# Optimization experiments

Measured on AMD Instinct MI355X. Metric: run time of the kernel, lower is better.

The kernel has to match this reference:

```python
import jax, jax.numpy as jnp
import numpy as np

B, D, E, H, O = 32768, 1200, 16, 1024, 1
K = 4
LN_EPS = 1e-5


def setup_inputs() -> dict:
    key = jax.random.key(0)
    ks = jax.random.split(key, 4)
    x = jax.random.normal(ks[0], (B, D), dtype=jnp.float32)
    w_gate = jax.random.normal(ks[1], (D, E), dtype=jnp.float32) * 0.05
    W1 = jax.random.normal(ks[2], (E, D, H), dtype=jnp.float32) * 0.02
    b1 = jnp.zeros((E, H), dtype=jnp.float32)
    gamma = jnp.ones((E, H), dtype=jnp.float32)
    beta = jnp.zeros((E, H), dtype=jnp.float32)
    W2 = jax.random.normal(ks[3], (E, H, O), dtype=jnp.float32) * 0.02
    b2 = jnp.zeros((E, O), dtype=jnp.float32)
    return {"x": x, "w_gate": w_gate, "W1": W1, "b1": b1,
            "gamma": gamma, "beta": beta, "W2": W2, "b2": b2, "k": K}


def _cv_squared(v):
    # torch .var() is unbiased (ddof=1)
    return jnp.var(v, ddof=1) / (jnp.mean(v) ** 2 + 1e-10)


def reference(x, w_gate, W1, b1, gamma, beta, W2, b2, k):
    nB = x.shape[0]
    nE = w_gate.shape[1]
    # --- top-k gating (eval path: no noise, dropout identity) ---
    logits = jax.nn.softmax(x @ w_gate, axis=1)               # [B, E]
    top_vals, top_idx = jax.lax.top_k(logits, min(k + 1, nE))  # [B, k+1]
    tk_v = top_vals[:, :k]                                     # [B, k]
    tk_i = top_idx[:, :k]
    tk_g = tk_v / (jnp.sum(tk_v, axis=1, keepdims=True) + 1e-6)
    gates = jnp.zeros_like(logits).at[jnp.arange(nB)[:, None], tk_i].set(tk_g)
    # --- load-balancing loss ---
    importance = gates.sum(0)
    load = (gates > 0).sum(0).astype(jnp.float32)
    loss = 0.5 * (_cv_squared(importance) + _cv_squared(load))
    # --- expert MLPs; dense per-expert compute masked by gates ---
    # (equivalent to sparse dispatch/combine: gate==0 rows contribute nothing,
    #  LayerNorm is per-row so no cross-token coupling)
    y = jnp.zeros((nB, W2.shape[-1]), dtype=jnp.float32)
    for e in range(nE):
        h = x @ W1[e] + b1[e]                                  # [B, H]
        mu = jnp.mean(h, axis=-1, keepdims=True)
        var = jnp.var(h, axis=-1, keepdims=True)               # biased, as torch LN
        h = (h - mu) / jnp.sqrt(var + LN_EPS) * gamma[e] + beta[e]
        h = jax.nn.relu(h)
        o = jax.nn.sigmoid(h @ W2[e] + b2[e])                  # [B, O]
        y = y + gates[:, e:e + 1] * o
    return y, loss
```

## Files before the change

kernel.cpp:

```cpp
#include <hip/hip_runtime.h>
#include <math.h>


#define B_SZ   32768
#define D_SZ   1200
#define DP     1216
#define E_SZ   16
#define H_SZ   1024
#define LN_EPS 1e-5f
#define BM     64
#define KBLK   32
#define NSTEP  (DP / KBLK)
#define NBG    512
#define GR     64

typedef __attribute__((ext_vector_type(8))) short  short8;
typedef __attribute__((ext_vector_type(4))) float  f32x4;

__device__ __forceinline__ unsigned short f2bf(float f) {
    unsigned u = __float_as_uint(f);
    unsigned r = u + 0x7FFFu + ((u >> 16) & 1u);
    return (unsigned short)(r >> 16);
}

__device__ __forceinline__ void gload_lds16(const void* g, void* l) {
    __builtin_amdgcn_global_load_lds(
        (const __attribute__((address_space(1))) void*)g,
        (__attribute__((address_space(3))) void*)l, 16, 0, 0);
}

__global__ __launch_bounds__(256)
void gate_a(const float* __restrict__ x, const float* __restrict__ wg,
            unsigned* __restrict__ tk_pack, float* __restrict__ gates4,
            unsigned short* __restrict__ lpos4,
            unsigned* __restrict__ hist_g, float* __restrict__ bimp_g)
{
    __shared__ int   hist[E_SZ];
    __shared__ float bimp[E_SZ];
    if (threadIdx.x < E_SZ) { hist[threadIdx.x] = 0; bimp[threadIdx.x] = 0.f; }
    __syncthreads();

    const int lane = threadIdx.x & 63;
    const int w    = threadIdx.x >> 6;
    const int rb   = blockIdx.x * GR;

    for (int it = 0; it < GR / 4; ++it) {
        const int row = rb + it * 4 + w;
        float acc[E_SZ];
#pragma unroll
        for (int e = 0; e < E_SZ; ++e) acc[e] = 0.f;

        const float* xr = x + (size_t)row * D_SZ;
        for (int d = lane; d < D_SZ; d += 64) {
            const float xv = xr[d];
            const float4* w4 = (const float4*)(wg + (size_t)d * E_SZ);
            const float4 a = w4[0], b = w4[1], c = w4[2], dd = w4[3];
            acc[0]  += xv * a.x;  acc[1]  += xv * a.y;
            acc[2]  += xv * a.z;  acc[3]  += xv * a.w;
            acc[4]  += xv * b.x;  acc[5]  += xv * b.y;
            acc[6]  += xv * b.z;  acc[7]  += xv * b.w;
            acc[8]  += xv * c.x;  acc[9]  += xv * c.y;
            acc[10] += xv * c.z;  acc[11] += xv * c.w;
            acc[12] += xv * dd.x; acc[13] += xv * dd.y;
            acc[14] += xv * dd.z; acc[15] += xv * dd.w;
        }
#pragma unroll
        for (int e = 0; e < E_SZ; ++e) {
            float v = acc[e];
            v += __shfl_xor(v, 1);  v += __shfl_xor(v, 2);
            v += __shfl_xor(v, 4);  v += __shfl_xor(v, 8);
            v += __shfl_xor(v, 16); v += __shfl_xor(v, 32);
            acc[e] = v;
        }
        if (lane == 0) {
            float mx = acc[0];
#pragma unroll
            for (int e = 1; e < E_SZ; ++e) mx = fmaxf(mx, acc[e]);
            float p[E_SZ]; float s = 0.f;
#pragma unroll
            for (int e = 0; e < E_SZ; ++e) { p[e] = expf(acc[e] - mx); s += p[e]; }
            const float inv = 1.f / s;

            unsigned msk = 0; int idx[4]; float val[4]; float gsum = 0.f;
#pragma unroll
            for (int tsel = 0; tsel < 4; ++tsel) {
                float bv = -1.f; int bi = 0;
#pragma unroll
                for (int e = 0; e < E_SZ; ++e) {
                    const bool ok = !((msk >> e) & 1u) && (p[e] > bv);
                    bv = ok ? p[e] : bv; bi = ok ? e : bi;
                }
                msk |= 1u << bi;
                idx[tsel] = bi; val[tsel] = bv * inv; gsum += bv * inv;
            }
            const float denom = gsum + 1e-6f;
            unsigned tkp = 0;
#pragma unroll
            for (int tsel = 0; tsel < 4; ++tsel) {
                const float g = val[tsel] / denom;
                const int e = idx[tsel];
                const int lp = atomicAdd(&hist[e], 1);
                atomicAdd(&bimp[e], g);
                tkp |= (unsigned)e << (8 * tsel);
                gates4[row * 4 + tsel] = g;
                lpos4[row * 4 + tsel]  = (unsigned short)lp;
            }
            tk_pack[row] = tkp;
        }
    }
    __syncthreads();
    if (threadIdx.x < E_SZ) {
        hist_g[blockIdx.x * E_SZ + threadIdx.x] = (unsigned)hist[threadIdx.x];
        bimp_g[blockIdx.x * E_SZ + threadIdx.x] = bimp[threadIdx.x];
    }
}

__global__ void gate_b(const unsigned* __restrict__ hist_g, const float* __restrict__ bimp_g,
                       unsigned* __restrict__ base_g, int* __restrict__ cnt,
                       float* __restrict__ imp, int* __restrict__ loadc,
                       float* __restrict__ loss_out)
{
    __shared__ float s_i[E_SZ], s_c[E_SZ];
    const int t = threadIdx.x;
    if (t < E_SZ) {
        unsigned run = 0; float ri = 0.f;
#pragma unroll 8
        for (int b = 0; b < NBG; ++b) {
            base_g[b * E_SZ + t] = run;
            run += hist_g[b * E_SZ + t];
            ri  += bimp_g[b * E_SZ + t];
        }
        cnt[t] = (int)run; imp[t] = ri; loadc[t] = (int)run;
        s_i[t] = ri; s_c[t] = (float)run;
    }
    __syncthreads();
    if (t == 0) {
        float mi = 0.f, ml = 0.f;
        for (int e = 0; e < E_SZ; ++e) { mi += s_i[e]; ml += s_c[e]; }
        mi *= (1.f / E_SZ); ml *= (1.f / E_SZ);
        float vi = 0.f, vl = 0.f;
        for (int e = 0; e < E_SZ; ++e) {
            const float di = s_i[e] - mi; vi += di * di;
            const float dl = s_c[e] - ml; vl += dl * dl;
        }
        vi *= (1.f / (E_SZ - 1)); vl *= (1.f / (E_SZ - 1));
        *loss_out = 0.5f * (vi / (mi * mi + 1e-10f) + vl / (ml * ml + 1e-10f));
    }
}

__global__ __launch_bounds__(256)
void gate_c(const unsigned* __restrict__ tk_pack, const float* __restrict__ gates4,
            const unsigned short* __restrict__ lpos4, const unsigned* __restrict__ base_g,
            int* __restrict__ bucket_row, float* __restrict__ bucket_gate)
{
    const int t   = threadIdx.x;
    const int row = blockIdx.x * GR + (t >> 2);
    const int j   = t & 3;
    const unsigned tkp = tk_pack[row];
    const int e = (int)((tkp >> (8 * j)) & 0xffu);
    const unsigned dst = base_g[blockIdx.x * E_SZ + e] + (unsigned)lpos4[row * 4 + j];
    bucket_row[e * B_SZ + dst]  = row;
    bucket_gate[e * B_SZ + dst] = gates4[row * 4 + j];
}

__global__ __launch_bounds__(256)
void pack_w1(const float* __restrict__ W1, unsigned short* __restrict__ Wp)
{
    __shared__ float tile[32][33];
    const int e  = blockIdx.z;
    const int d0 = blockIdx.x * 32;
    const int h0 = blockIdx.y * 32;
    const int tx = threadIdx.x & 31, ty = threadIdx.x >> 5;

    const float* W1e = W1 + (size_t)e * D_SZ * H_SZ;
#pragma unroll
    for (int i = 0; i < 4; ++i) {
        const int d = d0 + ty + i * 8;
        tile[ty + i * 8][tx] = (d < D_SZ) ? W1e[(size_t)d * H_SZ + h0 + tx] : 0.f;
    }
    __syncthreads();
    unsigned short* WpE = Wp + (size_t)e * H_SZ * DP;
#pragma unroll
    for (int i = 0; i < 4; ++i) {
        const int h = h0 + ty + i * 8;
        WpE[(size_t)h * DP + d0 + tx] = f2bf(tile[tx][ty + i * 8]);
    }
}

__global__ __launch_bounds__(1024, 4)
void expert_kernel(const float* __restrict__ x, const unsigned short* __restrict__ Wp,
                   const float* __restrict__ b1, const float* __restrict__ gamma,
                   const float* __restrict__ beta, const float* __restrict__ W2,
                   const float* __restrict__ b2,
                   const int* __restrict__ bucket_row,
                   const float* __restrict__ bucket_gate,
                   const int* __restrict__ cnt, float* __restrict__ y)
{
    const int e   = blockIdx.y;
    const int n_e = cnt[e];
    const int r0  = blockIdx.x * BM;
    if (r0 >= n_e) return;

    __shared__ unsigned short As[2][BM * KBLK];
    __shared__ unsigned short Bs[2][H_SZ * KBLK];
    __shared__ float red[16][BM][2];
    __shared__ float ln_m[BM], ln_r[BM];
    __shared__ int   srow[BM];
    __shared__ float sgate[BM];

    const int t   = threadIdx.x;
    const int w   = t >> 6;
    const int l   = t & 63;
    const int l15 = l & 15;
    const int lg  = l >> 4;
    const int sw  = (l15 >> 1) & 3;

    if (t < BM) {
        const int i = r0 + t;
        srow[t]  = (i < n_e) ? bucket_row[e * B_SZ + i] : -1;
        sgate[t] = (i < n_e) ? bucket_gate[e * B_SZ + i] : 0.f;
    }
    __syncthreads();

    const int ar = t >> 4;
    const int ai = t & 15;
    const int ak = ai * 2;
    const int abyte = ar * 64 + ((ai & 3) << 2) + ((((ai >> 2) ^ ((ar >> 1) & 3)) & 3) << 4);
    const int sr = srow[ar];
    const float* xrp = x + (size_t)(sr >= 0 ? sr : 0) * D_SZ;

    const unsigned short* WpE = Wp + (size_t)e * H_SZ * DP;
    const int bn0 = w * 64;
    const size_t bsrc = (size_t)(bn0 + (l >> 2)) * DP + (size_t)(((l & 3) ^ ((l >> 3) & 3)) * 8);

    f32x4 acc[16];
#pragma unroll
    for (int i = 0; i < 16; ++i) acc[i] = {0.f, 0.f, 0.f, 0.f};

    {
        float2 x0 = *(const float2*)(xrp + ak);
        ushort2 uv; uv.x = f2bf(x0.x); uv.y = f2bf(x0.y);
        *(ushort2*)((char*)&As[0][0] + abyte) = uv;
        unsigned short* Bn = &Bs[0][0];
#pragma unroll
        for (int i = 0; i < 4; ++i)
            gload_lds16(WpE + bsrc + (size_t)(i * 16) * DP, Bn + (bn0 + i * 16) * KBLK);
    }
    __syncthreads();

    int cur = 0;
    for (int step = 0; step < NSTEP; ++step) {
        const int  nxt  = cur ^ 1;
        const bool more = (step + 1) < NSTEP;
        float2 xn = {0.f, 0.f};
        if (more) {
            const int kk = (step + 1) * KBLK;
            if (kk + ak < D_SZ) xn = *(const float2*)(xrp + kk + ak);
            unsigned short* Bn = &Bs[nxt][0];
#pragma unroll
            for (int i = 0; i < 4; ++i)
                gload_lds16(WpE + bsrc + (size_t)(i * 16) * DP + kk,
                            Bn + (bn0 + i * 16) * KBLK);
        }
        const char* Ac = (const char*)&As[cur][0];
        const char* Bc = (const char*)&Bs[cur][0];
        short8 af[4], bfr[4];
#pragma unroll
        for (int m = 0; m < 4; ++m)
            af[m] = *(const short8*)(Ac + (m * 16 + l15) * 64 + ((lg ^ sw) << 4));
#pragma unroll
        for (int n = 0; n < 4; ++n)
            bfr[n] = *(const short8*)(Bc + (size_t)(bn0 + n * 16 + l15) * 64 + ((lg ^ sw) << 4));
#pragma unroll
        for (int m = 0; m < 4; ++m)
#pragma unroll
            for (int n = 0; n < 4; ++n)
                acc[m * 4 + n] = __builtin_amdgcn_mfma_f32_16x16x32_bf16(
                    af[m], bfr[n], acc[m * 4 + n], 0, 0, 0);
        if (more) {
            ushort2 uv; uv.x = f2bf(xn.x); uv.y = f2bf(xn.y);
            *(ushort2*)((char*)&As[nxt][0] + abyte) = uv;
        }
        __syncthreads();
        cur = nxt;
    }

    const float* b1e = b1    + (size_t)e * H_SZ;
    const float* gme = gamma + (size_t)e * H_SZ;
    const float* bte = beta  + (size_t)e * H_SZ;
    const float* w2e = W2    + (size_t)e * H_SZ;

    float b1v[4];
#pragma unroll
    for (int n = 0; n < 4; ++n) b1v[n] = b1e[bn0 + n * 16 + l15];

#pragma unroll
    for (int m = 0; m < 4; ++m) {
        float s[4], q[4];
#pragma unroll
        for (int j = 0; j < 4; ++j) {
            float sv = 0.f, qv = 0.f;
#pragma unroll
            for (int n = 0; n < 4; ++n) {
                const float v = acc[m * 4 + n][j] + b1v[n];
                acc[m * 4 + n][j] = v;
                sv += v; qv += v * v;
            }
            s[j] = sv; q[j] = qv;
        }
#pragma unroll
        for (int j = 0; j < 4; ++j) {
#pragma unroll
            for (int d = 1; d < 16; d <<= 1) {
                s[j] += __shfl_xor(s[j], d);
                q[j] += __shfl_xor(q[j], d);
            }
        }
        if (l15 == 0) {
#pragma unroll
            for (int j = 0; j < 4; ++j) {
                const int row = m * 16 + lg * 4 + j;
                red[w][row][0] = s[j]; red[w][row][1] = q[j];
            }
        }
    }
    __syncthreads();

    if (t < BM) {
        float s = 0.f, q = 0.f;
#pragma unroll
        for (int ww = 0; ww < 16; ++ww) { s += red[ww][t][0]; q += red[ww][t][1]; }
        const float mean = s * (1.f / H_SZ);
        const float var  = q * (1.f / H_SZ) - mean * mean;
        ln_m[t] = mean;
        ln_r[t] = 1.f / sqrtf(var + LN_EPS);
    }
    __syncthreads();

    float gmv[4], btv[4], w2v[4];
#pragma unroll
    for (int n = 0; n < 4; ++n) {
        const int col = bn0 + n * 16 + l15;
        gmv[n] = gme[col]; btv[n] = bte[col]; w2v[n] = w2e[col];
    }
#pragma unroll
    for (int m = 0; m < 4; ++m) {
        float p[4];
#pragma unroll
        for (int j = 0; j < 4; ++j) {
            const int row = m * 16 + lg * 4 + j;
            const float mm = ln_m[row], rr = ln_r[row];
            float pv = 0.f;
#pragma unroll
            for (int n = 0; n < 4; ++n) {
                float h = (acc[m * 4 + n][j] - mm) * rr * gmv[n] + btv[n];
                h = fmaxf(h, 0.f);
                pv += h * w2v[n];
            }
            p[j] = pv;
        }
#pragma unroll
        for (int j = 0; j < 4; ++j)
#pragma unroll
            for (int d = 1; d < 16; d <<= 1) p[j] += __shfl_xor(p[j], d);
        if (l15 == 0) {
#pragma unroll
            for (int j = 0; j < 4; ++j) red[w][m * 16 + lg * 4 + j][0] = p[j];
        }
    }
    __syncthreads();

    if (t < BM && srow[t] >= 0) {
        float z = b2[e];
#pragma unroll
        for (int ww = 0; ww < 16; ++ww) z += red[ww][t][0];
        const float o = 1.f / (1.f + expf(-z));
        atomicAdd(&y[srow[t]], sgate[t] * o);
    }
}

extern "C" void kernel_launch(void* const* d_in, const int* in_sizes, int n_in,
                              void* d_out, int out_size, void* d_ws, size_t ws_size,
                              hipStream_t stream)
{
    const float* x     = (const float*)d_in[0];
    const float* wg    = (const float*)d_in[1];
    const float* W1    = (const float*)d_in[2];
    const float* b1    = (const float*)d_in[3];
    const float* gamma = (const float*)d_in[4];
    const float* beta  = (const float*)d_in[5];
    const float* W2    = (const float*)d_in[6];
    const float* b2    = (const float*)d_in[7];
    float* y = (float*)d_out;

    char* ws = (char*)d_ws;
    int*   bucket_row  = (int*)ws;
    float* bucket_gate = (float*)(ws + (size_t)E_SZ * B_SZ * 4);
    const size_t base  = (size_t)E_SZ * B_SZ * 8;
    int*   cnt  = (int*)(ws + base);
    float* imp  = (float*)(ws + base + 64);
    int*   load = (int*)(ws + base + 128);
    unsigned short* Wp = (unsigned short*)(ws + base + 1024);

    char* g = ws + base + 1024;
    unsigned*       tk_pack = (unsigned*)g;
    float*          gates4  = (float*)(g + (size_t)B_SZ * 4);
    unsigned short* lpos4   = (unsigned short*)(g + (size_t)B_SZ * 20);
    unsigned*       hist_g  = (unsigned*)(g + (size_t)B_SZ * 28);
    float*          bimp_g  = (float*)(g + (size_t)B_SZ * 28 + NBG * E_SZ * 4);
    unsigned*       base_g  = (unsigned*)(g + (size_t)B_SZ * 28 + NBG * E_SZ * 8);

    hipMemsetAsync(d_out, 0, (size_t)B_SZ * sizeof(float), stream);

    gate_a<<<NBG, 256, 0, stream>>>(x, wg, tk_pack, gates4, lpos4, hist_g, bimp_g);
    gate_b<<<1, 64, 0, stream>>>(hist_g, bimp_g, base_g, cnt, imp, load, y + B_SZ);
    gate_c<<<NBG, 256, 0, stream>>>(tk_pack, gates4, lpos4, base_g, bucket_row, bucket_gate);
    pack_w1<<<dim3(DP / 32, H_SZ / 32, E_SZ), 256, 0, stream>>>(W1, Wp);
    expert_kernel<<<dim3(B_SZ / BM, E_SZ), 1024, 0, stream>>>(
        x, Wp, b1, gamma, beta, W2, b2, bucket_row, bucket_gate, cnt, y);
}
```

Baseline: 1.141 ms.

## Load A fragments from global and use per-wave B buffers without block barriers

gate_a now also writes a bf16 copy of x into the workspace when it has room. The expert GEMM then reads A fragments for its gathered rows straight from that copy, or converts fp32 on the fly if there is no room, instead of staging them in LDS. Each wave streams only its own slice of W1 into private double-buffered LDS. Since no wave reads another wave's slice, the per-step block barriers are replaced by vmcnt waits. gate_b now stages the histograms in LDS first, and the extra cost is a bf16 write of x plus A reads repeated by all 16 waves, relying on L2 hits.

```diff
diff --git a/kernel.cpp b/kernel.cpp
--- a/kernel.cpp
+++ b/kernel.cpp
@@ -31,6 +31,7 @@
 
 __global__ __launch_bounds__(256)
 void gate_a(const float* __restrict__ x, const float* __restrict__ wg,
+            unsigned short* __restrict__ xb,
             unsigned* __restrict__ tk_pack, float* __restrict__ gates4,
             unsigned short* __restrict__ lpos4,
             unsigned* __restrict__ hist_g, float* __restrict__ bimp_g)
@@ -53,6 +54,7 @@
         const float* xr = x + (size_t)row * D_SZ;
         for (int d = lane; d < D_SZ; d += 64) {
             const float xv = xr[d];
+            if (xb) xb[(size_t)row * D_SZ + d] = f2bf(xv);
             const float4* w4 = (const float4*)(wg + (size_t)d * E_SZ);
             const float4 a = w4[0], b = w4[1], c = w4[2], dd = w4[3];
             acc[0]  += xv * a.x;  acc[1]  += xv * a.y;
@@ -115,20 +117,24 @@
     }
 }
 
-__global__ void gate_b(const unsigned* __restrict__ hist_g, const float* __restrict__ bimp_g,
-                       unsigned* __restrict__ base_g, int* __restrict__ cnt,
-                       float* __restrict__ imp, int* __restrict__ loadc,
-                       float* __restrict__ loss_out)
-{
-    __shared__ float s_i[E_SZ], s_c[E_SZ];
+__global__ __launch_bounds__(1024)
+void gate_b(const unsigned* __restrict__ hist_g, const float* __restrict__ bimp_g,
+            unsigned* __restrict__ base_g, int* __restrict__ cnt,
+            float* __restrict__ imp, int* __restrict__ loadc,
+            float* __restrict__ loss_out)
+{
+    __shared__ unsigned hh[NBG * E_SZ];
+    __shared__ float    bb[NBG * E_SZ];
+    __shared__ float    s_i[E_SZ], s_c[E_SZ];
     const int t = threadIdx.x;
+    for (int i = t; i < NBG * E_SZ; i += 1024) { hh[i] = hist_g[i]; bb[i] = bimp_g[i]; }
+    __syncthreads();
     if (t < E_SZ) {
         unsigned run = 0; float ri = 0.f;
-#pragma unroll 8
         for (int b = 0; b < NBG; ++b) {
             base_g[b * E_SZ + t] = run;
-            run += hist_g[b * E_SZ + t];
-            ri  += bimp_g[b * E_SZ + t];
+            run += hh[b * E_SZ + t];
+            ri  += bb[b * E_SZ + t];
         }
         cnt[t] = (int)run; imp[t] = ri; loadc[t] = (int)run;
         s_i[t] = ri; s_c[t] = (float)run;
@@ -187,8 +193,10 @@
     }
 }
 
+template<int MODE>
 __global__ __launch_bounds__(1024, 4)
-void expert_kernel(const float* __restrict__ x, const unsigned short* __restrict__ Wp,
+void expert_kernel(const float* __restrict__ x, const unsigned short* __restrict__ xb,
+                   const unsigned short* __restrict__ Wp,
                    const float* __restrict__ b1, const float* __restrict__ gamma,
                    const float* __restrict__ beta, const float* __restrict__ W2,
                    const float* __restrict__ b2,
@@ -201,8 +209,7 @@
     const int r0  = blockIdx.x * BM;
     if (r0 >= n_e) return;
 
-    __shared__ unsigned short As[2][BM * KBLK];
-    __shared__ unsigned short Bs[2][H_SZ * KBLK];
+    __shared__ unsigned short Bs[2][16 * 64 * KBLK];
     __shared__ float red[16][BM][2];
     __shared__ float ln_m[BM], ln_r[BM];
     __shared__ int   srow[BM];
@@ -213,7 +220,6 @@
     const int l   = t & 63;
     const int l15 = l & 15;
     const int lg  = l >> 4;
-    const int sw  = (l15 >> 1) & 3;
 
     if (t < BM) {
         const int i = r0 + t;
@@ -222,68 +228,78 @@
     }
     __syncthreads();
 
-    const int ar = t >> 4;
-    const int ai = t & 15;
-    const int ak = ai * 2;
-    const int abyte = ar * 64 + ((ai & 3) << 2) + ((((ai >> 2) ^ ((ar >> 1) & 3)) & 3) << 4);
-    const int sr = srow[ar];
-    const float* xrp = x + (size_t)(sr >= 0 ? sr : 0) * D_SZ;
+    const unsigned short* pA[4];
+    const float*          pAx[4];
+#pragma unroll
+    for (int m = 0; m < 4; ++m) {
+        int rr = srow[m * 16 + l15]; rr = (rr >= 0) ? rr : 0;
+        if (MODE) pA[m]  = xb + (size_t)rr * D_SZ + lg * 8;
+        else      pAx[m] = x  + (size_t)rr * D_SZ + lg * 8;
+    }
 
     const unsigned short* WpE = Wp + (size_t)e * H_SZ * DP;
     const int bn0 = w * 64;
-    const size_t bsrc = (size_t)(bn0 + (l >> 2)) * DP + (size_t)(((l & 3) ^ ((l >> 3) & 3)) * 8);
+    unsigned short* Bw0 = &Bs[0][w * 2048];
+    unsigned short* Bw1 = &Bs[1][w * 2048];
+    const unsigned short* bsrc = WpE + (size_t)(bn0 + (l >> 2)) * DP + (l & 3) * 8;
 
     f32x4 acc[16];
 #pragma unroll
     for (int i = 0; i < 16; ++i) acc[i] = {0.f, 0.f, 0.f, 0.f};
 
-    {
-        float2 x0 = *(const float2*)(xrp + ak);
-        ushort2 uv; uv.x = f2bf(x0.x); uv.y = f2bf(x0.y);
-        *(ushort2*)((char*)&As[0][0] + abyte) = uv;
-        unsigned short* Bn = &Bs[0][0];
-#pragma unroll
-        for (int i = 0; i < 4; ++i)
-            gload_lds16(WpE + bsrc + (size_t)(i * 16) * DP, Bn + (bn0 + i * 16) * KBLK);
-    }
-    __syncthreads();
-
-    int cur = 0;
-    for (int step = 0; step < NSTEP; ++step) {
-        const int  nxt  = cur ^ 1;
-        const bool more = (step + 1) < NSTEP;
-        float2 xn = {0.f, 0.f};
-        if (more) {
-            const int kk = (step + 1) * KBLK;
-            if (kk + ak < D_SZ) xn = *(const float2*)(xrp + kk + ak);
-            unsigned short* Bn = &Bs[nxt][0];
-#pragma unroll
-            for (int i = 0; i < 4; ++i)
-                gload_lds16(WpE + bsrc + (size_t)(i * 16) * DP + kk,
-                            Bn + (bn0 + i * 16) * KBLK);
-        }
-        const char* Ac = (const char*)&As[cur][0];
-        const char* Bc = (const char*)&Bs[cur][0];
-        short8 af[4], bfr[4];
-#pragma unroll
-        for (int m = 0; m < 4; ++m)
-            af[m] = *(const short8*)(Ac + (m * 16 + l15) * 64 + ((lg ^ sw) << 4));
-#pragma unroll
-        for (int n = 0; n < 4; ++n)
-            bfr[n] = *(const short8*)(Bc + (size_t)(bn0 + n * 16 + l15) * 64 + ((lg ^ sw) << 4));
-#pragma unroll
-        for (int m = 0; m < 4; ++m)
-#pragma unroll
-            for (int n = 0; n < 4; ++n)
-                acc[m * 4 + n] = __builtin_amdgcn_mfma_f32_16x16x32_bf16(
-                    af[m], bfr[n], acc[m * 4 + n], 0, 0, 0);
-        if (more) {
-            ushort2 uv; uv.x = f2bf(xn.x); uv.y = f2bf(xn.y);
-            *(ushort2*)((char*)&As[nxt][0] + abyte) = uv;
-        }
-        __syncthreads();
-        cur = nxt;
-    }
+#pragma unroll
+    for (int i = 0; i < 4; ++i)
+        gload_lds16(bsrc + (size_t)(i * 16) * DP, Bw0 + i * 512);
+
+#define EXP_BODY(KB, BC, BN)                                                      \
+    {                                                                             \
+        asm volatile("s_waitcnt vmcnt(0)" ::: "memory");                          \
+        __builtin_amdgcn_sched_barrier(0);                                        \
+        const int kn_ = (KB) + KBLK;                                              \
+        if (kn_ < DP) {                                                           \
+            _Pragma("unroll")                                                     \
+            for (int i = 0; i < 4; ++i)                                           \
+                gload_lds16(bsrc + (size_t)(i * 16) * DP + kn_, (BN) + i * 512);  \
+        }                                                                         \
+        short8 af[4];                                                             \
+        if (MODE) {                                                               \
+            _Pragma("unroll")                                                     \
+            for (int m = 0; m < 4; ++m)                                           \
+                af[m] = *(const short8*)(pA[m] + (KB));                           \
+        } else {                                                                  \
+            const bool okg_ = ((KB) + lg * 8) < D_SZ;                             \
+            _Pragma("unroll")                                                     \
+            for (int m = 0; m < 4; ++m) {                                         \
+                if (okg_) {                                                       \
+                    float4 a0 = *(const float4*)(pAx[m] + (KB));                  \
+                    float4 a1 = *(const float4*)(pAx[m] + (KB) + 4);              \
+                    af[m][0] = (short)f2bf(a0.x); af[m][1] = (short)f2bf(a0.y);   \
+                    af[m][2] = (short)f2bf(a0.z); af[m][3] = (short)f2bf(a0.w);   \
+                    af[m][4] = (short)f2bf(a1.x); af[m][5] = (short)f2bf(a1.y);   \
+                    af[m][6] = (short)f2bf(a1.z); af[m][7] = (short)f2bf(a1.w);   \
+                } else {                                                          \
+                    af[m] = (short8){0,0,0,0,0,0,0,0};                            \
+                }                                                                 \
+            }                                                                     \
+        }                                                                         \
+        short8 bfr[4];                                                            \
+        _Pragma("unroll")                                                         \
+        for (int n = 0; n < 4; ++n)                                               \
+            bfr[n] = *(const short8*)&(BC)[(n * 16 + l15) * 32 + lg * 8];         \
+        _Pragma("unroll")                                                         \
+        for (int m = 0; m < 4; ++m)                                               \
+            _Pragma("unroll")                                                     \
+            for (int n = 0; n < 4; ++n)                                           \
+                acc[m * 4 + n] = __builtin_amdgcn_mfma_f32_16x16x32_bf16(         \
+                    af[m], bfr[n], acc[m * 4 + n], 0, 0, 0);                      \
+    }
+
+#pragma unroll 1
+    for (int kb = 0; kb < DP; kb += 2 * KBLK) {
+        EXP_BODY(kb,        Bw0, Bw1)
+        EXP_BODY(kb + KBLK, Bw1, Bw0)
+    }
+#undef EXP_BODY
 
     const float* b1e = b1    + (size_t)e * H_SZ;
     const float* gme = gamma + (size_t)e * H_SZ;
@@ -401,6 +417,13 @@
     float* imp  = (float*)(ws + base + 64);
     int*   load = (int*)(ws + base + 128);
     unsigned short* Wp = (unsigned short*)(ws + base + 1024);
+    const size_t WPB = (size_t)E_SZ * H_SZ * DP * 2;
+
+    size_t off_xb = base + 1024 + WPB;
+    off_xb = (off_xb + 255) & ~(size_t)255;
+    const size_t need = off_xb + (size_t)B_SZ * D_SZ * 2 + 256;
+    const bool use_xb = (ws_size >= need);
+    unsigned short* xb = use_xb ? (unsigned short*)(ws + off_xb) : nullptr;
 
     char* g = ws + base + 1024;
     unsigned*       tk_pack = (unsigned*)g;
@@ -412,10 +435,14 @@
 
     hipMemsetAsync(d_out, 0, (size_t)B_SZ * sizeof(float), stream);
 
-    gate_a<<<NBG, 256, 0, stream>>>(x, wg, tk_pack, gates4, lpos4, hist_g, bimp_g);
-    gate_b<<<1, 64, 0, stream>>>(hist_g, bimp_g, base_g, cnt, imp, load, y + B_SZ);
+    gate_a<<<NBG, 256, 0, stream>>>(x, wg, xb, tk_pack, gates4, lpos4, hist_g, bimp_g);
+    gate_b<<<1, 1024, 0, stream>>>(hist_g, bimp_g, base_g, cnt, imp, load, y + B_SZ);
     gate_c<<<NBG, 256, 0, stream>>>(tk_pack, gates4, lpos4, base_g, bucket_row, bucket_gate);
     pack_w1<<<dim3(DP / 32, H_SZ / 32, E_SZ), 256, 0, stream>>>(W1, Wp);
-    expert_kernel<<<dim3(B_SZ / BM, E_SZ), 1024, 0, stream>>>(
-        x, Wp, b1, gamma, beta, W2, b2, bucket_row, bucket_gate, cnt, y);
-}
+    if (use_xb)
+        expert_kernel<1><<<dim3(B_SZ / BM, E_SZ), 1024, 0, stream>>>(
+            x, xb, Wp, b1, gamma, beta, W2, b2, bucket_row, bucket_gate, cnt, y);
+    else
+        expert_kernel<0><<<dim3(B_SZ / BM, E_SZ), 1024, 0, stream>>>(
+            x, nullptr, Wp, b1, gamma, beta, W2, b2, bucket_row, bucket_gate, cnt, y);
+}
```

New measurement: 1.370 ms. 1.2x slower.
